# Performance work log

Hardware: AMD Instinct MI355X
Metric: run time of the kernel (lower is better)

## Reference

```python
import jax, jax.numpy as jnp
import numpy as np

B, H, W, C = 8, 256, 256, 128  # batch, grid-H, grid-W, channel width
MODES = 16
SCALE = 1.0 / (C * C)  # 1/(in_width*out_width)


def _corner_mask(h, w, f):
    # mask truncates the FIRST two axes of w_ft (as in the original code),
    # keeping the full rfft axis.
    m = np.zeros((h, w, f), dtype=np.float32)
    m[:MODES, :MODES, :] = 1.0
    m[-MODES:, :MODES, :] = 1.0
    m[:MODES, -MODES:, :] = 1.0
    m[-MODES:, -MODES:, :] = 1.0
    return jnp.asarray(m)


def setup_inputs() -> dict:
    key = jax.random.key(0)
    k1, k2 = jax.random.split(key)
    x = jax.random.normal(k1, (B, H, W, C), dtype=jnp.float32)
    w = SCALE * jax.random.uniform(k2, (H, W, C), dtype=jnp.float32)
    b = jnp.zeros((H, W, C), dtype=jnp.float32)
    return {"x": x, "w": w, "b": b}


def reference(x, w, b):
    # rfft2d over the innermost two dims (W, C), matching tf.signal.rfft2d
    x_ft = jnp.fft.rfft2(x, axes=(-2, -1))   # [B, H, W, C//2+1] complex
    w_ft = jnp.fft.rfft2(w, axes=(-2, -1))   # [H, W, C//2+1]
    b_ft = jnp.fft.rfft2(b, axes=(-2, -1))
    xw_ft = x_ft * w_ft + b_ft               # broadcast over batch
    mask = _corner_mask(*w_ft.shape)         # corners along axes (0,1)
    xw_ft = xw_ft * mask
    # irfft2d with default sizes recovers last dim = 2*(C//2+1-1) = C
    return jnp.fft.irfft2(xw_ft, axes=(-2, -1))
```

## Files before the change

kernel.cpp:

```cpp
#include <hip/hip_runtime.h>

#define TPK 512
#define TPA 1024

typedef float f4v __attribute__((ext_vector_type(4)));

__device__ __forceinline__ int br7(int k) {
  return (int)(__brev((unsigned int)k) >> 25);
}

template <int NT>
__device__ __forceinline__ void zero_fill_slab(float* __restrict__ out,
                                               int zi, int tid) {
  const int zb = zi / 224;
  const int zh = 16 + (zi - zb * 224);
  f4v* o4 = (f4v*)(out + ((size_t)(zb * 256 + zh)) * 32768);
  const f4v z = {0.f, 0.f, 0.f, 0.f};
  #pragma unroll 4
  for (int i = tid; i < 8192; i += NT)
    __builtin_nontemporal_store(z, &o4[i]);
}

__device__ __forceinline__ void fft16_pos(float* ar, float* ai) {
  constexpr float TC[4][8] = {
    {1.f, 0.f, 0.f, 0.f, 0.f, 0.f, 0.f, 0.f},
    {1.f, 0.f, 0.f, 0.f, 0.f, 0.f, 0.f, 0.f},
    {1.f, 0.70710678f, 0.f, -0.70710678f, 0.f, 0.f, 0.f, 0.f},
    {1.f, 0.92387953f, 0.70710678f, 0.38268343f, 0.f, -0.38268343f, -0.70710678f, -0.92387953f}
  };
  constexpr float TS[4][8] = {
    {0.f, 0.f, 0.f, 0.f, 0.f, 0.f, 0.f, 0.f},
    {0.f, 1.f, 0.f, 0.f, 0.f, 0.f, 0.f, 0.f},
    {0.f, 0.70710678f, 1.f, 0.70710678f, 0.f, 0.f, 0.f, 0.f},
    {0.f, 0.38268343f, 0.70710678f, 0.92387953f, 1.f, 0.92387953f, 0.70710678f, 0.38268343f}
  };
  #pragma unroll
  for (int s = 0; s < 4; ++s) {
    const int L = 1 << s;
    #pragma unroll
    for (int jj = 0; jj < 8; ++jj) {
      if (jj < L) {
        const float tc = TC[s][jj], ts = TS[s][jj];
        #pragma unroll
        for (int i0 = jj; i0 < 16; i0 += 2 * L) {
          const float xr = ar[i0 + L], xi = ai[i0 + L];
          const float pr = xr * tc - xi * ts;
          const float pi = xr * ts + xi * tc;
          const float qr = ar[i0], qi = ai[i0];
          ar[i0 + L] = qr - pr; ai[i0 + L] = qi - pi;
          ar[i0]     = qr + pr; ai[i0]     = qi + pi;
        }
      }
    }
  }
}

template <int TPBv>
__device__ void forward_slab(const float* __restrict__ src,
                             float (*XR)[128], float (*XI)[128],
                             float (*SR)[128], float (*SI)[128],
                             const float* Rc, const float* Rs, int tid) {
  constexpr int NQ = TPBv / 128;
  constexpr int JN = 16 / NQ;
  const int c = tid & 127;
  const int q = tid >> 7;

  constexpr float C16[16] = {1.f, 0.92387953f, 0.70710678f, 0.38268343f, 0.f,
                             -0.38268343f, -0.70710678f, -0.92387953f, -1.f,
                             -0.92387953f, -0.70710678f, -0.38268343f, 0.f,
                             0.38268343f, 0.70710678f, 0.92387953f};
  constexpr float S16[16] = {0.f, 0.38268343f, 0.70710678f, 0.92387953f, 1.f,
                             0.92387953f, 0.70710678f, 0.38268343f, 0.f,
                             -0.38268343f, -0.70710678f, -0.92387953f, -1.f,
                             -0.92387953f, -0.70710678f, -0.38268343f};

  float accR[17], accI[17];
  #pragma unroll
  for (int f = 0; f < 17; ++f) { accR[f] = 0.f; accI[f] = 0.f; }

  #pragma unroll
  for (int j = 0; j < JN; ++j) {
    const int w0 = q * JN + j;
    float xv[16];
    #pragma unroll
    for (int w1 = 0; w1 < 16; ++w1)
      xv[w1] = src[(w1 * 16 + w0) * 128 + c];
    float SRe[9], SIm[9];
    #pragma unroll
    for (int g = 0; g < 9; ++g) {
      float sr = 0.f, si = 0.f;
      #pragma unroll
      for (int w1 = 0; w1 < 16; ++w1) {
        const int m = (g * w1) & 15;
        sr = fmaf(xv[w1], C16[m], sr);
        si = fmaf(xv[w1], -S16[m], si);
      }
      SRe[g] = sr; SIm[g] = si;
    }
    #pragma unroll
    for (int f = 0; f < 17; ++f) {
      const int g = f & 15;
      const float sr = (g <= 8) ? SRe[g] : SRe[16 - g];
      const float si = (g <= 8) ? SIm[g] : -SIm[16 - g];
      const int idx = (f * w0) & 255;
      const float tc = Rc[idx], ts = -Rs[idx];
      accR[f] = fmaf(sr, tc, fmaf(-si, ts, accR[f]));
      accI[f] = fmaf(sr, ts, fmaf(si, tc, accI[f]));
    }
  }
  #pragma unroll
  for (int r = 0; r < NQ / 2; ++r) {
    if (q == 2 * r) {
      if (r == 0) {
        #pragma unroll
        for (int f = 0; f < 17; ++f) { XR[f][c] = accR[f]; XI[f][c] = accI[f]; }
      } else {
        #pragma unroll
        for (int f = 0; f < 17; ++f) { XR[f][c] += accR[f]; XI[f][c] += accI[f]; }
      }
    } else if (q == 2 * r + 1) {
      if (r == 0) {
        #pragma unroll
        for (int f = 0; f < 17; ++f) { SR[f][c] = accR[f]; SI[f][c] = accI[f]; }
      } else {
        #pragma unroll
        for (int f = 0; f < 17; ++f) { SR[f][c] += accR[f]; SI[f][c] += accI[f]; }
      }
    }
    __syncthreads();
  }
  for (int u = tid; u < 17 * 128; u += TPBv) {
    const int row = u >> 7, cc = u & 127;
    XR[row][cc] += SR[row][cc];
    XI[row][cc] += SI[row][cc];
  }
  __syncthreads();

  for (int s = 6; s >= 0; --s) {
    const int L = 1 << s;
    for (int u = tid; u < 17 * 64; u += TPBv) {
      const int row = u >> 6, qq = u & 63;
      const int jj = qq & (L - 1);
      const int pos = ((qq >> s) << (s + 1)) | jj;
      const int ti = jj << (7 - s);
      const float tc = Rc[ti], ts = Rs[ti];
      const float a0r = XR[row][pos],     a0i = XI[row][pos];
      const float b0r = XR[row][pos + L], b0i = XI[row][pos + L];
      XR[row][pos] = a0r + b0r; XI[row][pos] = a0i + b0i;
      const float dr = a0r - b0r, di = a0i - b0i;
      XR[row][pos + L] = fmaf(dr, tc, di * ts);
      XI[row][pos + L] = fmaf(di, tc, -dr * ts);
    }
    __syncthreads();
  }
}

__global__ __launch_bounds__(TPK) void k0_wft_and_fill(
    const float* __restrict__ wp, const float* __restrict__ bp,
    float2* __restrict__ wsW, float2* __restrict__ wsB,
    float* __restrict__ out) {
  const int bid = blockIdx.x;
  const int tid = threadIdx.x;
  if (bid >= 64) {
    zero_fill_slab<TPK>(out, bid - 64, tid);
    return;
  }
  __shared__ float XR[17][128], XI[17][128];
  __shared__ float SR[17][128], SI[17][128];
  __shared__ float Rc[256], Rs[256];
  for (int i = tid; i < 256; i += TPK) {
    float sv, cv; sincosf(6.283185307179586f * (float)i / 256.0f, &sv, &cv);
    Rc[i] = cv; Rs[i] = sv;
  }
  __syncthreads();
  const int which = bid >> 5;
  const int ha = bid & 31;
  const int h = (ha < 16) ? ha : (224 + ha);
  const float* src = (which ? bp : wp) + (size_t)h * 32768;
  forward_slab<TPK>(src, XR, XI, SR, SI, Rc, Rs, tid);
  float2* dst = which ? wsB : wsW;
  for (int u = tid; u < 32 * 65; u += TPK) {
    const int fi = u / 65, k = u - fi * 65;
    const int f = fi - 16;
    float xr, xi;
    if (f >= 0) { const int p = br7(k); xr = XR[f][p]; xi = XI[f][p]; }
    else { const int kk = (128 - k) & 127; const int p = br7(kk);
           xr = XR[-f][p]; xi = -XI[-f][p]; }
    dst[(ha * 32 + fi) * 65 + k] = make_float2(xr, xi);
  }
}

__global__ __launch_bounds__(TPA) void fourier_active(
    const float* __restrict__ x, const float2* __restrict__ wsW,
    const float2* __restrict__ wsB, float* __restrict__ out) {
  const int bid = blockIdx.x;
  const int tid = threadIdx.x;
  __shared__ float XR[17][128], XI[17][128];
  __shared__ float TR[32][128], TI[32][128];
  __shared__ float Rc[256], Rs[256];
  for (int i = tid; i < 256; i += TPA) {
    float sv, cv; sincosf(6.283185307179586f * (float)i / 256.0f, &sv, &cv);
    Rc[i] = cv; Rs[i] = sv;
  }
  __syncthreads();

  const int b = bid >> 5;
  const int ha = bid & 31;
  const int h = (ha < 16) ? ha : (224 + ha);
  const float* src = x + ((size_t)(b * 256 + h)) * 32768;
  forward_slab<TPA>(src, XR, XI, (float(*)[128])TR, (float(*)[128])TI,
                    Rc, Rs, tid);

  for (int u = tid; u < 32 * 128; u += TPA) {
    const int fi = u >> 7, k = u & 127;
    float gr = 0.f, gi = 0.f;
    if (k <= 64) {
      const int f = fi - 16;
      float xr, xi;
      if (f >= 0) { const int p = br7(k); xr = XR[f][p]; xi = XI[f][p]; }
      else { const int kk = (128 - k) & 127; const int p = br7(kk);
             xr = XR[-f][p]; xi = -XI[-f][p]; }
      const float2 wf = wsW[(ha * 32 + fi) * 65 + k];
      const float2 bf = wsB[(ha * 32 + fi) * 65 + k];
      gr = xr * wf.x - xi * wf.y + bf.x;
      gi = xr * wf.y + xi * wf.x + bf.y;
      const float al = (k == 0 || k == 64) ? 1.f : 2.f;
      gr *= al; gi *= al;
    }
    const int p = br7(k);
    TR[fi][p] = gr; TI[fi][p] = gi;
  }
  __syncthreads();

  for (int s = 0; s <= 6; ++s) {
    const int L = 1 << s;
    for (int u = tid; u < 32 * 64; u += TPA) {
      const int row = u >> 6, qq = u & 63;
      const int jj = qq & (L - 1);
      const int pos = ((qq >> s) << (s + 1)) | jj;
      const int ti = jj << (7 - s);
      const float tc = Rc[ti], ts = Rs[ti];
      const float b0r = TR[row][pos + L], b0i = TI[row][pos + L];
      const float pr = b0r * tc - b0i * ts;
      const float pi = fmaf(b0r, ts, b0i * tc);
      const float a0r = TR[row][pos], a0i = TI[row][pos];
      TR[row][pos + L] = a0r - pr; TI[row][pos + L] = a0i - pi;
      TR[row][pos]     = a0r + pr; TI[row][pos]     = a0i + pi;
    }
    __syncthreads();
  }

  const int c = tid & 127;
  const int q = tid >> 7;
  constexpr int BR4[16] = {0, 8, 4, 12, 2, 10, 6, 14, 1, 9, 5, 13, 3, 11, 7, 15};
  const float inv = 1.0f / 32768.0f;
  float* og = out + ((size_t)(b * 256 + h)) * 32768;

  #pragma unroll 1
  for (int it = 0; it < 2; ++it) {
    const int w0 = q + it * 8;
    float Ur[16], Ui[16];
    #pragma unroll
    for (int g = 0; g < 16; ++g) {
      const int gb = BR4[g];
      const float t1r = TR[gb + 16][c], t1i = TI[gb + 16][c];
      const float t0r = TR[gb][c],      t0i = TI[gb][c];
      const int i1 = (gb * w0) & 255;
      const int i2 = ((gb - 16) * w0) & 255;
      const float c1 = Rc[i1], s1 = Rs[i1];
      const float c2 = Rc[i2], s2 = Rs[i2];
      Ur[g] = t1r * c1 - t1i * s1 + t0r * c2 - t0i * s2;
      Ui[g] = t1r * s1 + t1i * c1 + t0r * s2 + t0i * c2;
    }
    fft16_pos(Ur, Ui);
    #pragma unroll
    for (int w1 = 0; w1 < 16; ++w1)
      og[(w1 * 16 + w0) * 128 + c] = Ur[w1] * inv;
  }
}

extern "C" void kernel_launch(void* const* d_in, const int* in_sizes, int n_in,
                              void* d_out, int out_size, void* d_ws, size_t ws_size,
                              hipStream_t stream) {
  const float* x = (const float*)d_in[0];
  const float* w = (const float*)d_in[1];
  const float* b = (const float*)d_in[2];
  float* out = (float*)d_out;
  float2* wsW = (float2*)d_ws;
  float2* wsB = wsW + 32 * 32 * 65;

  hipLaunchKernelGGL(k0_wft_and_fill, dim3(64 + 1792), dim3(TPK), 0, stream,
                     w, b, wsW, wsB, out);
  hipLaunchKernelGGL(fourier_active, dim3(256), dim3(TPA), 0, stream,
                     x, wsW, wsB, out);
}
```

Before: 73.29 us.

## Replace LDS-staged 128-point FFT stages with wavefront shuffle butterflies

In the active kernel, the forward 128-point column FFT and the inverse 128-point FFT now run one row per wavefront, each lane holding two elements. Butterflies exchange data with __shfl_xor instead of shared memory, which removes about a dozen block-wide __syncthreads and the LDS round trips per stage. The spectral multiply is fused into the same per-wavefront pass. The weight kernel keeps the LDS path through a split helper. The cost is extra select and shuffle instructions, and with 16 wavefronts covering 17 rows, one wavefront does a second row, so the load is uneven.

```diff
diff --git a/kernel.cpp b/kernel.cpp
--- a/kernel.cpp
+++ b/kernel.cpp
@@ -56,10 +56,10 @@
 }
 
 template <int TPBv>
-__device__ void forward_slab(const float* __restrict__ src,
-                             float (*XR)[128], float (*XI)[128],
-                             float (*SR)[128], float (*SI)[128],
-                             const float* Rc, const float* Rs, int tid) {
+__device__ void phaseA_reduce(const float* __restrict__ src,
+                              float (*XR)[128], float (*XI)[128],
+                              float (*SR)[128], float (*SI)[128],
+                              const float* Rc, const float* Rs, int tid) {
   constexpr int NQ = TPBv / 128;
   constexpr int JN = 16 / NQ;
   const int c = tid & 127;
@@ -135,7 +135,11 @@
     XI[row][cc] += SI[row][cc];
   }
   __syncthreads();
-
+}
+
+template <int TPBv>
+__device__ void fftc17_lds(float (*XR)[128], float (*XI)[128],
+                           const float* Rc, const float* Rs, int tid) {
   for (int s = 6; s >= 0; --s) {
     const int L = 1 << s;
     for (int u = tid; u < 17 * 64; u += TPBv) {
@@ -177,7 +181,8 @@
   const int ha = bid & 31;
   const int h = (ha < 16) ? ha : (224 + ha);
   const float* src = (which ? bp : wp) + (size_t)h * 32768;
-  forward_slab<TPK>(src, XR, XI, SR, SI, Rc, Rs, tid);
+  phaseA_reduce<TPK>(src, XR, XI, SR, SI, Rc, Rs, tid);
+  fftc17_lds<TPK>(XR, XI, Rc, Rs, tid);
   float2* dst = which ? wsB : wsW;
   for (int u = tid; u < 32 * 65; u += TPK) {
     const int fi = u / 65, k = u - fi * 65;
@@ -208,47 +213,110 @@
   const int ha = bid & 31;
   const int h = (ha < 16) ? ha : (224 + ha);
   const float* src = x + ((size_t)(b * 256 + h)) * 32768;
-  forward_slab<TPA>(src, XR, XI, (float(*)[128])TR, (float(*)[128])TI,
-                    Rc, Rs, tid);
-
-  for (int u = tid; u < 32 * 128; u += TPA) {
-    const int fi = u >> 7, k = u & 127;
-    float gr = 0.f, gi = 0.f;
-    if (k <= 64) {
-      const int f = fi - 16;
-      float xr, xi;
-      if (f >= 0) { const int p = br7(k); xr = XR[f][p]; xi = XI[f][p]; }
-      else { const int kk = (128 - k) & 127; const int p = br7(kk);
-             xr = XR[-f][p]; xi = -XI[-f][p]; }
-      const float2 wf = wsW[(ha * 32 + fi) * 65 + k];
-      const float2 bf = wsB[(ha * 32 + fi) * 65 + k];
-      gr = xr * wf.x - xi * wf.y + bf.x;
-      gi = xr * wf.y + xi * wf.x + bf.y;
-      const float al = (k == 0 || k == 64) ? 1.f : 2.f;
-      gr *= al; gi *= al;
-    }
-    const int p = br7(k);
-    TR[fi][p] = gr; TI[fi][p] = gi;
-  }
-  __syncthreads();
-
-  for (int s = 0; s <= 6; ++s) {
-    const int L = 1 << s;
-    for (int u = tid; u < 32 * 64; u += TPA) {
-      const int row = u >> 6, qq = u & 63;
-      const int jj = qq & (L - 1);
-      const int pos = ((qq >> s) << (s + 1)) | jj;
-      const int ti = jj << (7 - s);
-      const float tc = Rc[ti], ts = Rs[ti];
-      const float b0r = TR[row][pos + L], b0i = TI[row][pos + L];
-      const float pr = b0r * tc - b0i * ts;
-      const float pi = fmaf(b0r, ts, b0i * tc);
-      const float a0r = TR[row][pos], a0i = TI[row][pos];
-      TR[row][pos + L] = a0r - pr; TI[row][pos + L] = a0i - pi;
-      TR[row][pos]     = a0r + pr; TI[row][pos]     = a0i + pi;
-    }
-    __syncthreads();
-  }
+  phaseA_reduce<TPA>(src, XR, XI, (float(*)[128])TR, (float(*)[128])TI,
+                     Rc, Rs, tid);
+
+  const int wid = tid >> 6, lane = tid & 63;
+  const int i0 = lane, i1 = lane + 64;
+
+  for (int row = wid; row < 17; row += 16) {
+    float ar0 = XR[row][i0], ai0 = XI[row][i0];
+    float ar1 = XR[row][i1], ai1 = XI[row][i1];
+    {
+      const float tc = Rc[2 * lane], ts = Rs[2 * lane];
+      const float sr = ar0 - ar1, si = ai0 - ai1;
+      ar0 += ar1; ai0 += ai1;
+      ar1 = fmaf(sr, tc,  si * ts);
+      ai1 = fmaf(si, tc, -sr * ts);
+    }
+    #pragma unroll
+    for (int s = 5; s >= 0; --s) {
+      const int L = 1 << s;
+      const int m2 = (lane & (L - 1)) << (7 - s);
+      const float wc = Rc[m2], wsn = Rs[m2];
+      const bool hi = (lane & L) != 0;
+      const float br0 = __shfl_xor(ar0, L), bi0 = __shfl_xor(ai0, L);
+      const float br1 = __shfl_xor(ar1, L), bi1 = __shfl_xor(ai1, L);
+      float dr0 = hi ? (br0 - ar0) : (ar0 + br0);
+      float di0 = hi ? (bi0 - ai0) : (ai0 + bi0);
+      float dr1 = hi ? (br1 - ar1) : (ar1 + br1);
+      float di1 = hi ? (bi1 - ai1) : (ai1 + bi1);
+      if (hi) {
+        const float t0 = fmaf(dr0, wc,  di0 * wsn);
+        di0 = fmaf(di0, wc, -dr0 * wsn); dr0 = t0;
+        const float t1 = fmaf(dr1, wc,  di1 * wsn);
+        di1 = fmaf(di1, wc, -dr1 * wsn); dr1 = t1;
+      }
+      ar0 = dr0; ai0 = di0; ar1 = dr1; ai1 = di1;
+    }
+    XR[row][i0] = ar0; XI[row][i0] = ai0;
+    XR[row][i1] = ar1; XI[row][i1] = ai1;
+  }
+  __syncthreads();
+
+  const int k0 = br7(i0);
+  const int k1 = k0 + 1;
+  #pragma unroll
+  for (int rr = 0; rr < 2; ++rr) {
+    int fi; float xr0, xi0, xr1, xi1;
+    if (rr == 0) {
+      fi = wid + 16;
+      xr0 = XR[wid][i0]; xi0 = XI[wid][i0];
+      xr1 = XR[wid][i1]; xi1 = XI[wid][i1];
+    } else {
+      fi = wid;
+      const int mrow = 16 - wid;
+      const int pm0 = br7((128 - k0) & 127);
+      const int pm1 = br7((128 - k1) & 127);
+      xr0 = XR[mrow][pm0]; xi0 = -XI[mrow][pm0];
+      xr1 = XR[mrow][pm1]; xi1 = -XI[mrow][pm1];
+    }
+    float gr0 = 0.f, gi0 = 0.f, gr1 = 0.f, gi1 = 0.f;
+    const float2* wrow = &wsW[(ha * 32 + fi) * 65];
+    const float2* brow = &wsB[(ha * 32 + fi) * 65];
+    if (k0 <= 64) {
+      const float2 wf = wrow[k0], bf = brow[k0];
+      const float al = (k0 == 0 || k0 == 64) ? 1.f : 2.f;
+      gr0 = al * (xr0 * wf.x - xi0 * wf.y + bf.x);
+      gi0 = al * (xr0 * wf.y + xi0 * wf.x + bf.y);
+    }
+    if (k1 <= 64) {
+      const float2 wf = wrow[k1], bf = brow[k1];
+      gr1 = 2.f * (xr1 * wf.x - xi1 * wf.y + bf.x);
+      gi1 = 2.f * (xr1 * wf.y + xi1 * wf.x + bf.y);
+    }
+    #pragma unroll
+    for (int s = 0; s <= 5; ++s) {
+      const int L = 1 << s;
+      const int m2 = (lane & (L - 1)) << (7 - s);
+      const float wc = Rc[m2], wsn = Rs[m2];
+      const bool hi = (lane & L) != 0;
+      const float br0 = __shfl_xor(gr0, L), bi0 = __shfl_xor(gi0, L);
+      const float br1 = __shfl_xor(gr1, L), bi1 = __shfl_xor(gi1, L);
+      const float q0ri = hi ? gr0 : br0, q0ii = hi ? gi0 : bi0;
+      const float q1ri = hi ? gr1 : br1, q1ii = hi ? gi1 : bi1;
+      const float q0r = fmaf(q0ri, wc, -q0ii * wsn);
+      const float q0i = fmaf(q0ii, wc,  q0ri * wsn);
+      const float q1r = fmaf(q1ri, wc, -q1ii * wsn);
+      const float q1i = fmaf(q1ii, wc,  q1ri * wsn);
+      const float p0r = hi ? br0 : gr0, p0i = hi ? bi0 : gi0;
+      const float p1r = hi ? br1 : gr1, p1i = hi ? bi1 : gi1;
+      gr0 = hi ? (p0r - q0r) : (p0r + q0r);
+      gi0 = hi ? (p0i - q0i) : (p0i + q0i);
+      gr1 = hi ? (p1r - q1r) : (p1r + q1r);
+      gi1 = hi ? (p1i - q1i) : (p1i + q1i);
+    }
+    {
+      const float wc = Rc[2 * lane], wsn = Rs[2 * lane];
+      const float qr = fmaf(gr1, wc, -gi1 * wsn);
+      const float qi = fmaf(gi1, wc,  gr1 * wsn);
+      gr1 = gr0 - qr; gi1 = gi0 - qi;
+      gr0 = gr0 + qr; gi0 = gi0 + qi;
+    }
+    TR[fi][i0] = gr0; TI[fi][i0] = gi0;
+    TR[fi][i1] = gr1; TI[fi][i1] = gi1;
+  }
+  __syncthreads();
 
   const int c = tid & 127;
   const int q = tid >> 7;
@@ -265,10 +333,10 @@
       const int gb = BR4[g];
       const float t1r = TR[gb + 16][c], t1i = TI[gb + 16][c];
       const float t0r = TR[gb][c],      t0i = TI[gb][c];
-      const int i1 = (gb * w0) & 255;
-      const int i2 = ((gb - 16) * w0) & 255;
-      const float c1 = Rc[i1], s1 = Rs[i1];
-      const float c2 = Rc[i2], s2 = Rs[i2];
+      const int iw1 = (gb * w0) & 255;
+      const int iw2 = ((gb - 16) * w0) & 255;
+      const float c1 = Rc[iw1], s1 = Rs[iw1];
+      const float c2 = Rc[iw2], s2 = Rs[iw2];
       Ur[g] = t1r * c1 - t1i * s1 + t0r * c2 - t0i * s2;
       Ui[g] = t1r * s1 + t1i * c1 + t0r * s2 + t0i * c2;
     }
```

New measurement: 71.43 us. 2.5% less time.

## Interleave zero-fill stores into active kernel FFT stages and prefetch weights

Applied to the files above, without the earlier changes.

Moves most of the zero-fill work (1280 of 1792 slabs) out of the first kernel and spreads it as nontemporal stores across the FFT barrier stages of the active kernel. The goal is to overlap memory-bound zero writes with the LDS-bound FFT work. Weight and bias spectra are prefetched into registers before the column FFT, and the barriers become explicit lgkmcnt waits so outstanding global stores do not block them. The trade-offs are more register pressure in the 1024-thread kernel, a tighter launch-bounds hint, and a first kernel that now does much less work.

```diff
diff --git a/kernel.cpp b/kernel.cpp
--- a/kernel.cpp
+++ b/kernel.cpp
@@ -2,12 +2,34 @@
 
 #define TPK 512
 #define TPA 1024
+#define NF0 512
+#define FPB 5
+#define NST (FPB * 8)
 
 typedef float f4v __attribute__((ext_vector_type(4)));
 
 __device__ __forceinline__ int br7(int k) {
   return (int)(__brev((unsigned int)k) >> 25);
 }
+
+__device__ __forceinline__ void bar_lds() {
+  asm volatile("s_waitcnt lgkmcnt(0)\ns_barrier" ::: "memory");
+}
+
+#define FILL3(PT)                                                           \
+  {                                                                         \
+    _Pragma("unroll")                                                       \
+    for (int _j = 0; _j < 3; ++_j) {                                        \
+      const int _idx = 3 * (PT) + _j;                                       \
+      if (_idx < NST) {                                                     \
+        const int _zi = NF0 + bid * FPB + (_idx >> 3);                      \
+        const int _zb = _zi / 224;                                          \
+        const int _zh = 16 + (_zi - _zb * 224);                             \
+        f4v* _o4 = (f4v*)(out + ((size_t)(_zb * 256 + _zh)) * 32768);       \
+        __builtin_nontemporal_store(z, &_o4[tid + ((_idx & 7) << 10)]);     \
+      }                                                                     \
+    }                                                                       \
+  }
 
 template <int NT>
 __device__ __forceinline__ void zero_fill_slab(float* __restrict__ out,
@@ -56,10 +78,10 @@
 }
 
 template <int TPBv>
-__device__ void forward_slab(const float* __restrict__ src,
-                             float (*XR)[128], float (*XI)[128],
-                             float (*SR)[128], float (*SI)[128],
-                             const float* Rc, const float* Rs, int tid) {
+__device__ void phaseA_reduce(const float* __restrict__ src,
+                              float (*XR)[128], float (*XI)[128],
+                              float (*SR)[128], float (*SI)[128],
+                              const float* Rc, const float* Rs, int tid) {
   constexpr int NQ = TPBv / 128;
   constexpr int JN = 16 / NQ;
   const int c = tid & 127;
@@ -135,7 +157,11 @@
     XI[row][cc] += SI[row][cc];
   }
   __syncthreads();
-
+}
+
+template <int TPBv>
+__device__ void fftc17_lds(float (*XR)[128], float (*XI)[128],
+                           const float* Rc, const float* Rs, int tid) {
   for (int s = 6; s >= 0; --s) {
     const int L = 1 << s;
     for (int u = tid; u < 17 * 64; u += TPBv) {
@@ -177,7 +203,8 @@
   const int ha = bid & 31;
   const int h = (ha < 16) ? ha : (224 + ha);
   const float* src = (which ? bp : wp) + (size_t)h * 32768;
-  forward_slab<TPK>(src, XR, XI, SR, SI, Rc, Rs, tid);
+  phaseA_reduce<TPK>(src, XR, XI, SR, SI, Rc, Rs, tid);
+  fftc17_lds<TPK>(XR, XI, Rc, Rs, tid);
   float2* dst = which ? wsB : wsW;
   for (int u = tid; u < 32 * 65; u += TPK) {
     const int fi = u / 65, k = u - fi * 65;
@@ -190,7 +217,7 @@
   }
 }
 
-__global__ __launch_bounds__(TPA) void fourier_active(
+__global__ __launch_bounds__(TPA, 4) void fourier_active(
     const float* __restrict__ x, const float2* __restrict__ wsW,
     const float2* __restrict__ wsB, float* __restrict__ out) {
   const int bid = blockIdx.x;
@@ -208,10 +235,47 @@
   const int ha = bid & 31;
   const int h = (ha < 16) ? ha : (224 + ha);
   const float* src = x + ((size_t)(b * 256 + h)) * 32768;
-  forward_slab<TPA>(src, XR, XI, (float(*)[128])TR, (float(*)[128])TI,
-                    Rc, Rs, tid);
-
-  for (int u = tid; u < 32 * 128; u += TPA) {
+  phaseA_reduce<TPA>(src, XR, XI, (float(*)[128])TR, (float(*)[128])TI,
+                     Rc, Rs, tid);
+
+  float wfx[4], wfy[4], bfx[4], bfy[4];
+  #pragma unroll
+  for (int t = 0; t < 4; ++t) {
+    const int u = tid + t * TPA;
+    const int fi = u >> 7, k = u & 127;
+    if (k <= 64) {
+      const float2 wf = wsW[(ha * 32 + fi) * 65 + k];
+      const float2 bf = wsB[(ha * 32 + fi) * 65 + k];
+      wfx[t] = wf.x; wfy[t] = wf.y; bfx[t] = bf.x; bfy[t] = bf.y;
+    } else { wfx[t] = 0.f; wfy[t] = 0.f; bfx[t] = 0.f; bfy[t] = 0.f; }
+  }
+  __builtin_amdgcn_sched_barrier(0);
+
+  const f4v z = {0.f, 0.f, 0.f, 0.f};
+
+  #pragma unroll
+  for (int s = 6; s >= 0; --s) {
+    const int L = 1 << s;
+    for (int u = tid; u < 17 * 64; u += TPA) {
+      const int row = u >> 6, qq = u & 63;
+      const int jj = qq & (L - 1);
+      const int pos = ((qq >> s) << (s + 1)) | jj;
+      const int ti = jj << (7 - s);
+      const float tc = Rc[ti], ts = Rs[ti];
+      const float a0r = XR[row][pos],     a0i = XI[row][pos];
+      const float b0r = XR[row][pos + L], b0i = XI[row][pos + L];
+      XR[row][pos] = a0r + b0r; XI[row][pos] = a0i + b0i;
+      const float dr = a0r - b0r, di = a0i - b0i;
+      XR[row][pos + L] = fmaf(dr, tc, di * ts);
+      XI[row][pos + L] = fmaf(di, tc, -dr * ts);
+    }
+    FILL3(6 - s);
+    bar_lds();
+  }
+
+  #pragma unroll
+  for (int t = 0; t < 4; ++t) {
+    const int u = tid + t * TPA;
     const int fi = u >> 7, k = u & 127;
     float gr = 0.f, gi = 0.f;
     if (k <= 64) {
@@ -220,18 +284,18 @@
       if (f >= 0) { const int p = br7(k); xr = XR[f][p]; xi = XI[f][p]; }
       else { const int kk = (128 - k) & 127; const int p = br7(kk);
              xr = XR[-f][p]; xi = -XI[-f][p]; }
-      const float2 wf = wsW[(ha * 32 + fi) * 65 + k];
-      const float2 bf = wsB[(ha * 32 + fi) * 65 + k];
-      gr = xr * wf.x - xi * wf.y + bf.x;
-      gi = xr * wf.y + xi * wf.x + bf.y;
+      gr = xr * wfx[t] - xi * wfy[t] + bfx[t];
+      gi = xr * wfy[t] + xi * wfx[t] + bfy[t];
       const float al = (k == 0 || k == 64) ? 1.f : 2.f;
       gr *= al; gi *= al;
     }
     const int p = br7(k);
     TR[fi][p] = gr; TI[fi][p] = gi;
   }
-  __syncthreads();
-
+  FILL3(7);
+  bar_lds();
+
+  #pragma unroll
   for (int s = 0; s <= 6; ++s) {
     const int L = 1 << s;
     for (int u = tid; u < 32 * 64; u += TPA) {
@@ -247,7 +311,8 @@
       TR[row][pos + L] = a0r - pr; TI[row][pos + L] = a0i - pi;
       TR[row][pos]     = a0r + pr; TI[row][pos]     = a0i + pi;
     }
-    __syncthreads();
+    FILL3(8 + s);
+    bar_lds();
   }
 
   const int c = tid & 127;
@@ -265,10 +330,10 @@
       const int gb = BR4[g];
       const float t1r = TR[gb + 16][c], t1i = TI[gb + 16][c];
       const float t0r = TR[gb][c],      t0i = TI[gb][c];
-      const int i1 = (gb * w0) & 255;
-      const int i2 = ((gb - 16) * w0) & 255;
-      const float c1 = Rc[i1], s1 = Rs[i1];
-      const float c2 = Rc[i2], s2 = Rs[i2];
+      const int iw1 = (gb * w0) & 255;
+      const int iw2 = ((gb - 16) * w0) & 255;
+      const float c1 = Rc[iw1], s1 = Rs[iw1];
+      const float c2 = Rc[iw2], s2 = Rs[iw2];
       Ur[g] = t1r * c1 - t1i * s1 + t0r * c2 - t0i * s2;
       Ui[g] = t1r * s1 + t1i * c1 + t0r * s2 + t0i * c2;
     }
@@ -289,7 +354,7 @@
   float2* wsW = (float2*)d_ws;
   float2* wsB = wsW + 32 * 32 * 65;
 
-  hipLaunchKernelGGL(k0_wft_and_fill, dim3(64 + 1792), dim3(TPK), 0, stream,
+  hipLaunchKernelGGL(k0_wft_and_fill, dim3(64 + NF0), dim3(TPK), 0, stream,
                      w, b, wsW, wsB, out);
   hipLaunchKernelGGL(fourier_active, dim3(256), dim3(TPA), 0, stream,
                      x, wsW, wsB, out);
```

Result: faster. 69.08 us (-5.7%).

## Split zero-fill between kernels and fold Hermitian symmetry into forward DFT

Applied to the files above, without the earlier changes.

Moves most of the zero-fill of non-corner output slabs from the first kernel into the second, so those store-only blocks run alongside the active FFT blocks instead of serialising before them. The forward DFT stage now accumulates each conjugate pair of frequencies straight from the 9 computed half-spectrum sums, dropping the intermediate arrays and select logic. Minor tweaks: a fully unrolled zero-fill loop, unroll 2 on the outer loop, and a launch bound hint of 8. The 1024-thread zero-fill blocks in the second kernel may compete with the active blocks for occupancy.

```diff
diff --git a/kernel.cpp b/kernel.cpp
--- a/kernel.cpp
+++ b/kernel.cpp
@@ -2,6 +2,8 @@
 
 #define TPK 512
 #define TPA 1024
+#define NF0 448
+#define NACT 256
 
 typedef float f4v __attribute__((ext_vector_type(4)));
 
@@ -16,9 +18,9 @@
   const int zh = 16 + (zi - zb * 224);
   f4v* o4 = (f4v*)(out + ((size_t)(zb * 256 + zh)) * 32768);
   const f4v z = {0.f, 0.f, 0.f, 0.f};
-  #pragma unroll 4
-  for (int i = tid; i < 8192; i += NT)
-    __builtin_nontemporal_store(z, &o4[i]);
+  #pragma unroll
+  for (int i = 0; i < 8192 / NT; ++i)
+    __builtin_nontemporal_store(z, &o4[tid + i * NT]);
 }
 
 __device__ __forceinline__ void fft16_pos(float* ar, float* ai) {
@@ -56,10 +58,10 @@
 }
 
 template <int TPBv>
-__device__ void forward_slab(const float* __restrict__ src,
-                             float (*XR)[128], float (*XI)[128],
-                             float (*SR)[128], float (*SI)[128],
-                             const float* Rc, const float* Rs, int tid) {
+__device__ void phaseA_reduce(const float* __restrict__ src,
+                              float (*XR)[128], float (*XI)[128],
+                              float (*SR)[128], float (*SI)[128],
+                              const float* Rc, const float* Rs, int tid) {
   constexpr int NQ = TPBv / 128;
   constexpr int JN = 16 / NQ;
   const int c = tid & 127;
@@ -78,16 +80,15 @@
   #pragma unroll
   for (int f = 0; f < 17; ++f) { accR[f] = 0.f; accI[f] = 0.f; }
 
-  #pragma unroll
+  #pragma unroll 2
   for (int j = 0; j < JN; ++j) {
     const int w0 = q * JN + j;
     float xv[16];
     #pragma unroll
     for (int w1 = 0; w1 < 16; ++w1)
       xv[w1] = src[(w1 * 16 + w0) * 128 + c];
-    float SRe[9], SIm[9];
-    #pragma unroll
-    for (int g = 0; g < 9; ++g) {
+    #pragma unroll
+    for (int g = 0; g <= 8; ++g) {
       float sr = 0.f, si = 0.f;
       #pragma unroll
       for (int w1 = 0; w1 < 16; ++w1) {
@@ -95,17 +96,24 @@
         sr = fmaf(xv[w1], C16[m], sr);
         si = fmaf(xv[w1], -S16[m], si);
       }
-      SRe[g] = sr; SIm[g] = si;
-    }
-    #pragma unroll
-    for (int f = 0; f < 17; ++f) {
-      const int g = f & 15;
-      const float sr = (g <= 8) ? SRe[g] : SRe[16 - g];
-      const float si = (g <= 8) ? SIm[g] : -SIm[16 - g];
-      const int idx = (f * w0) & 255;
-      const float tc = Rc[idx], ts = -Rs[idx];
-      accR[f] = fmaf(sr, tc, fmaf(-si, ts, accR[f]));
-      accI[f] = fmaf(sr, ts, fmaf(si, tc, accI[f]));
+      {
+        const int idx = (g * w0) & 255;
+        const float rc = Rc[idx], rs = Rs[idx];
+        accR[g] = fmaf(sr, rc, fmaf(si, rs, accR[g]));
+        accI[g] = fmaf(si, rc, fmaf(-sr, rs, accI[g]));
+      }
+      if (g == 0) {
+        const int idx = (16 * w0) & 255;
+        const float rc = Rc[idx], rs = Rs[idx];
+        accR[16] = fmaf(sr, rc, fmaf(si, rs, accR[16]));
+        accI[16] = fmaf(si, rc, fmaf(-sr, rs, accI[16]));
+      } else if (g <= 7) {
+        const int f2 = 16 - g;
+        const int idx = (f2 * w0) & 255;
+        const float rc = Rc[idx], rs = Rs[idx];
+        accR[f2] = fmaf(sr, rc, fmaf(-si, rs, accR[f2]));
+        accI[f2] = fmaf(-si, rc, fmaf(-sr, rs, accI[f2]));
+      }
     }
   }
   #pragma unroll
@@ -135,7 +143,11 @@
     XI[row][cc] += SI[row][cc];
   }
   __syncthreads();
-
+}
+
+template <int TPBv>
+__device__ void fftc17_lds(float (*XR)[128], float (*XI)[128],
+                           const float* Rc, const float* Rs, int tid) {
   for (int s = 6; s >= 0; --s) {
     const int L = 1 << s;
     for (int u = tid; u < 17 * 64; u += TPBv) {
@@ -177,7 +189,8 @@
   const int ha = bid & 31;
   const int h = (ha < 16) ? ha : (224 + ha);
   const float* src = (which ? bp : wp) + (size_t)h * 32768;
-  forward_slab<TPK>(src, XR, XI, SR, SI, Rc, Rs, tid);
+  phaseA_reduce<TPK>(src, XR, XI, SR, SI, Rc, Rs, tid);
+  fftc17_lds<TPK>(XR, XI, Rc, Rs, tid);
   float2* dst = which ? wsB : wsW;
   for (int u = tid; u < 32 * 65; u += TPK) {
     const int fi = u / 65, k = u - fi * 65;
@@ -190,11 +203,15 @@
   }
 }
 
-__global__ __launch_bounds__(TPA) void fourier_active(
+__global__ __launch_bounds__(TPA, 8) void fourier_main(
     const float* __restrict__ x, const float2* __restrict__ wsW,
     const float2* __restrict__ wsB, float* __restrict__ out) {
   const int bid = blockIdx.x;
   const int tid = threadIdx.x;
+  if (bid >= NACT) {
+    zero_fill_slab<TPA>(out, NF0 + (bid - NACT), tid);
+    return;
+  }
   __shared__ float XR[17][128], XI[17][128];
   __shared__ float TR[32][128], TI[32][128];
   __shared__ float Rc[256], Rs[256];
@@ -208,8 +225,10 @@
   const int ha = bid & 31;
   const int h = (ha < 16) ? ha : (224 + ha);
   const float* src = x + ((size_t)(b * 256 + h)) * 32768;
-  forward_slab<TPA>(src, XR, XI, (float(*)[128])TR, (float(*)[128])TI,
-                    Rc, Rs, tid);
+  phaseA_reduce<TPA>(src, XR, XI, (float(*)[128])TR, (float(*)[128])TI,
+                     Rc, Rs, tid);
+
+  fftc17_lds<TPA>(XR, XI, Rc, Rs, tid);
 
   for (int u = tid; u < 32 * 128; u += TPA) {
     const int fi = u >> 7, k = u & 127;
@@ -265,10 +284,10 @@
       const int gb = BR4[g];
       const float t1r = TR[gb + 16][c], t1i = TI[gb + 16][c];
       const float t0r = TR[gb][c],      t0i = TI[gb][c];
-      const int i1 = (gb * w0) & 255;
-      const int i2 = ((gb - 16) * w0) & 255;
-      const float c1 = Rc[i1], s1 = Rs[i1];
-      const float c2 = Rc[i2], s2 = Rs[i2];
+      const int iw1 = (gb * w0) & 255;
+      const int iw2 = ((gb - 16) * w0) & 255;
+      const float c1 = Rc[iw1], s1 = Rs[iw1];
+      const float c2 = Rc[iw2], s2 = Rs[iw2];
       Ur[g] = t1r * c1 - t1i * s1 + t0r * c2 - t0i * s2;
       Ui[g] = t1r * s1 + t1i * c1 + t0r * s2 + t0i * c2;
     }
@@ -289,8 +308,8 @@
   float2* wsW = (float2*)d_ws;
   float2* wsB = wsW + 32 * 32 * 65;
 
-  hipLaunchKernelGGL(k0_wft_and_fill, dim3(64 + 1792), dim3(TPK), 0, stream,
+  hipLaunchKernelGGL(k0_wft_and_fill, dim3(64 + NF0), dim3(TPK), 0, stream,
                      w, b, wsW, wsB, out);
-  hipLaunchKernelGGL(fourier_active, dim3(256), dim3(TPA), 0, stream,
-                     x, wsW, wsB, out);
-}
+  hipLaunchKernelGGL(fourier_main, dim3(NACT + (1792 - NF0)), dim3(TPA), 0,
+                     stream, x, wsW, wsB, out);
+}
```

New measurement: 105.9 us. 1.44x slower.
